# Performance work log

Measured on AMD Instinct MI355X. Metric: run time of the kernel, lower is better.

The kernel has to match this reference:

```python
import jax, jax.numpy as jnp
import numpy as np

B, S, D, H = 8, 4096, 1024, 16
HD = D // H          # 64 head dim
NR = HD // 2         # 32 rotations
BASE = 10000.0


def setup_inputs() -> dict:
    key = jax.random.key(0)
    k0, k1, k2 = jax.random.split(key, 3)
    x = jax.random.normal(k0, (B, S, D), jnp.float32)
    thetas = jax.random.normal(k1, (NR,), jnp.float32) * 0.1
    r_pairs = jax.random.uniform(k2, (NR, 2), jnp.float32) * HD  # float indices in [0, HD)
    theta_scale = jnp.ones((1,), jnp.float32)
    n_rots_scale = jnp.ones((1,), jnp.float32)
    r_matrix = jnp.eye(HD, dtype=jnp.float32)
    inv_freq = 1.0 / (BASE ** (jnp.arange(0, HD, 2, dtype=jnp.float32) / HD))  # [HD/2]
    return {"x": x, "thetas": thetas, "r_pairs": r_pairs,
            "theta_scale": theta_scale, "n_rots_scale": n_rots_scale,
            "r_matrix": r_matrix, "inv_freq": inv_freq}


def reference(x, thetas, r_pairs, theta_scale, n_rots_scale, r_matrix, inv_freq):
    b, s, d = x.shape
    hd = r_matrix.shape[0]
    h = d // hd
    xf = x.reshape(-1, hd)  # [B*S*H, hd]

    # adjusted_n_rots = round(n_rots_scale * n_rots); n_rots_scale == 1 -> all rotations
    # (the int() in torch is non-differentiable/static anyway)
    idx = r_pairs.astype(jnp.int32)          # floor of non-negative floats, like .long()
    th = thetas * theta_scale[0]             # [NR]

    def step(xc, inp):
        i, j, t = inp
        c, sn = jnp.cos(t), jnp.sin(t)
        xi = xc[:, i]
        xj = xc[:, j]
        same = i == j
        # x @ G: col i -> xi*c + xj*s, col j -> -xi*s + xj*c; if i==j torch's
        # overwrite order leaves G[i,i] = cos -> col i = xi*c
        ni = jnp.where(same, xi * c, xi * c + xj * sn)
        nj = jnp.where(same, xi * c, -xi * sn + xj * c)
        xc = xc.at[:, i].set(ni)
        xc = xc.at[:, j].set(nj)
        return xc, None

    xf, _ = jax.lax.scan(step, xf, (idx[:, 0], idx[:, 1], th))
    xf = xf @ r_matrix                       # [B*S*H, hd]
    x4 = xf.reshape(b, s, h, hd)

    pos = jnp.arange(s, dtype=jnp.float32)
    sinusoid = pos[:, None] * inv_freq[None, :]        # [S, hd/2]
    sin = jnp.sin(sinusoid)[None, :, None, :]
    cos = jnp.cos(sinusoid)[None, :, None, :]
    x1 = x4[..., ::2]
    x2 = x4[..., 1::2]
    out = jnp.concatenate([x1 * cos - x2 * sin, x1 * sin + x2 * cos], axis=-1)
    return out.reshape(b, s, d)
```

## Files before the change

### kernel.cpp

```cpp
#include <hip/hip_runtime.h>

#define BB 8
#define SS 4096
#define DD 1024
#define HH 16
#define HD 64
#define NR 32
#define NROWS (BB * SS * HH)
#define NGRP (NROWS / 16)
#define GPW 4
#define GPB (4 * GPW)
#define NBLK (NGRP / GPB)

typedef __attribute__((ext_vector_type(8))) short bf16x8;
typedef __attribute__((ext_vector_type(4))) float f32x4;

__global__ __launch_bounds__(256) void build_pack_kernel(
    const float* __restrict__ thetas,
    const float* __restrict__ r_pairs,
    const float* __restrict__ theta_scale,
    const float* __restrict__ r_matrix,
    unsigned short* __restrict__ Apack)
{
    __shared__ float W[64 * 68];
    __shared__ int   ii[NR], jj[NR];
    __shared__ float cc[NR], ssn[NR];

    const int t = threadIdx.x;

#pragma unroll
    for (int it = 0; it < 16; ++it) {
        int idx = t + 256 * it;
        W[(idx >> 6) * 68 + (idx & 63)] = r_matrix[idx];
    }
    if (t < NR) {
        ii[t] = (int)r_pairs[2 * t];
        jj[t] = (int)r_pairs[2 * t + 1];
        float th = thetas[t] * theta_scale[0];
        cc[t]  = cosf(th);
        ssn[t] = sinf(th);
    }
    __syncthreads();

    if (t < 64) {
        for (int k = NR - 1; k >= 0; --k) {
            int i = ii[k], j = jj[k];
            float c = cc[k], s = ssn[k];
            float xi = W[i * 68 + t];
            float xj = W[j * 68 + t];
            if (i == j) {
                W[i * 68 + t] = c * xi;
            } else {
                W[i * 68 + t] = c * xi - s * xj;
                W[j * 68 + t] = s * xi + c * xj;
            }
        }
    }
    __syncthreads();

#pragma unroll
    for (int it = 0; it < 16; ++it) {
        int flat = t + 256 * it;
        int j    = flat & 7;
        int lane = (flat >> 3) & 63;
        int ks   = (flat >> 9) & 1;
        int tt   = flat >> 10;
        int i    = tt * 16 + (lane & 15);
        int k    = ks * 32 + ((lane >> 4) << 3) + j;
        float v  = W[k * 68 + i];
        unsigned u  = __float_as_uint(v);
        unsigned uh = u & 0xFFFF0000u;
        float fl    = v - __uint_as_float(uh);
        Apack[flat]        = (unsigned short)(uh >> 16);
        Apack[4096 + flat] = (unsigned short)(__float_as_uint(fl) >> 16);
    }
}

__device__ __forceinline__ void split8(const float4 a, const float4 b,
                                       bf16x8& hi, bf16x8& lo)
{
    const float f[8] = {a.x, a.y, a.z, a.w, b.x, b.y, b.z, b.w};
#pragma unroll
    for (int j = 0; j < 8; ++j) {
        unsigned u  = __float_as_uint(f[j]);
        unsigned uh = u & 0xFFFF0000u;
        hi[j] = (short)(uh >> 16);
        float fl = f[j] - __uint_as_float(uh);
        lo[j] = (short)(__float_as_uint(fl) >> 16);
    }
}

__global__ __launch_bounds__(256, 3) void rope_mfma_kernel(
    const float* __restrict__ x,
    const unsigned short* __restrict__ Apack,
    const float* __restrict__ inv_freq,
    float* __restrict__ out)
{
    const int lane = threadIdx.x & 63;
    const int wv   = threadIdx.x >> 6;
    const int q    = lane >> 4;
    const int rr   = lane & 15;

    bf16x8 Ah[4][2], Al[4][2];
    {
        const bf16x8* Ap = (const bf16x8*)Apack;
#pragma unroll
        for (int tt = 0; tt < 4; ++tt)
#pragma unroll
            for (int ks = 0; ks < 2; ++ks) {
                Ah[tt][ks] = Ap[(tt * 2 + ks) * 64 + lane];
                Al[tt][ks] = Ap[512 + (tt * 2 + ks) * 64 + lane];
            }
    }
    float2 invf[4];
#pragma unroll
    for (int tt = 0; tt < 4; ++tt)
        invf[tt] = *(const float2*)&inv_freq[tt * 8 + q * 2];

    int g = blockIdx.x * GPB + wv * GPW;

    const float* xr = x + ((size_t)g * 16 + rr) * 64 + q * 8;
    float4 fa0 = *(const float4*)(xr);
    float4 fa1 = *(const float4*)(xr + 4);
    float4 fa2 = *(const float4*)(xr + 32);
    float4 fa3 = *(const float4*)(xr + 36);

#pragma unroll 1
    for (int gi = 0; gi < GPW; ++gi, ++g) {
        float4 fb0 = fa0, fb1 = fa1, fb2 = fa2, fb3 = fa3;
        if (gi + 1 < GPW) {
            const float* xn = x + ((size_t)(g + 1) * 16 + rr) * 64 + q * 8;
            fb0 = *(const float4*)(xn);
            fb1 = *(const float4*)(xn + 4);
            fb2 = *(const float4*)(xn + 32);
            fb3 = *(const float4*)(xn + 36);
        }

        bf16x8 Bh0, Bl0, Bh1, Bl1;
        split8(fa0, fa1, Bh0, Bl0);
        split8(fa2, fa3, Bh1, Bl1);

        f32x4 acc[4];
#pragma unroll
        for (int tt = 0; tt < 4; ++tt) {
            f32x4 a = {0.f, 0.f, 0.f, 0.f};
            a = __builtin_amdgcn_mfma_f32_16x16x32_bf16(Ah[tt][0], Bh0, a, 0, 0, 0);
            a = __builtin_amdgcn_mfma_f32_16x16x32_bf16(Ah[tt][1], Bh1, a, 0, 0, 0);
            a = __builtin_amdgcn_mfma_f32_16x16x32_bf16(Al[tt][0], Bh0, a, 0, 0, 0);
            a = __builtin_amdgcn_mfma_f32_16x16x32_bf16(Al[tt][1], Bh1, a, 0, 0, 0);
            a = __builtin_amdgcn_mfma_f32_16x16x32_bf16(Ah[tt][0], Bl0, a, 0, 0, 0);
            a = __builtin_amdgcn_mfma_f32_16x16x32_bf16(Ah[tt][1], Bl1, a, 0, 0, 0);
            acc[tt] = a;
        }

        const float pos = (float)(g & (SS - 1));
        float* orow = out + ((size_t)g * 16 + rr) * 64;
#pragma unroll
        for (int tt = 0; tt < 4; ++tt) {
            float sn0, cs0, sn1, cs1;
            __sincosf(pos * invf[tt].x, &sn0, &cs0);
            __sincosf(pos * invf[tt].y, &sn1, &cs1);
            const float y0 = acc[tt][0], y1 = acc[tt][1];
            const float y2 = acc[tt][2], y3 = acc[tt][3];
            const int m0 = tt * 8 + q * 2;
            float2 o1 = { y0 * cs0 - y1 * sn0, y2 * cs1 - y3 * sn1 };
            float2 o2 = { y0 * sn0 + y1 * cs0, y2 * sn1 + y3 * cs1 };
            *(float2*)&orow[m0]      = o1;
            *(float2*)&orow[32 + m0] = o2;
        }

        fa0 = fb0; fa1 = fb1; fa2 = fb2; fa3 = fb3;
    }
}

extern "C" void kernel_launch(void* const* d_in, const int* in_sizes, int n_in,
                              void* d_out, int out_size, void* d_ws, size_t ws_size,
                              hipStream_t stream)
{
    const float* x           = (const float*)d_in[0];
    const float* thetas      = (const float*)d_in[1];
    const float* r_pairs     = (const float*)d_in[2];
    const float* theta_scale = (const float*)d_in[3];
    const float* r_matrix    = (const float*)d_in[5];
    const float* inv_freq    = (const float*)d_in[6];
    float* out = (float*)d_out;
    unsigned short* Apack = (unsigned short*)d_ws;

    build_pack_kernel<<<1, 256, 0, stream>>>(thetas, r_pairs, theta_scale,
                                             r_matrix, Apack);
    rope_mfma_kernel<<<NBLK, 256, 0, stream>>>(x, Apack, inv_freq, out);
}
```

Before: 259.4 us.

## Exchange MFMA outputs across lanes to emit 16-byte nontemporal stores

Lanes in adjacent quads swap accumulator values with a cross-lane shuffle, so each lane holds four consecutive output pairs and writes float4 stores instead of float2 stores. The stores are marked nontemporal to avoid cache pollution on this streaming output, and the occupancy hint rises from 3 to 4 blocks per CU. This halves the number of store instructions and widens each one, at the cost of shuffles and possible register pressure under the tighter launch bound.

Measured after the change: 264.3 us. Within noise of the previous version (+1.9%).

```diff
diff --git a/kernel.cpp b/kernel.cpp
--- a/kernel.cpp
+++ b/kernel.cpp
@@ -90,7 +90,7 @@
     }
 }
 
-__global__ __launch_bounds__(256, 3) void rope_mfma_kernel(
+__global__ __launch_bounds__(256, 4) void rope_mfma_kernel(
     const float* __restrict__ x,
     const unsigned short* __restrict__ Apack,
     const float* __restrict__ inv_freq,
@@ -100,6 +100,9 @@
     const int wv   = threadIdx.x >> 6;
     const int q    = lane >> 4;
     const int rr   = lane & 15;
+    const int qlo  = q & 1;
+    const int qhi  = q >> 1;
+    const bool odd = qlo != 0;
 
     bf16x8 Ah[4][2], Al[4][2];
     {
@@ -112,10 +115,10 @@
                 Al[tt][ks] = Ap[512 + (tt * 2 + ks) * 64 + lane];
             }
     }
-    float2 invf[4];
-#pragma unroll
-    for (int tt = 0; tt < 4; ++tt)
-        invf[tt] = *(const float2*)&inv_freq[tt * 8 + q * 2];
+    float4 invf4[2];
+#pragma unroll
+    for (int pr = 0; pr < 2; ++pr)
+        invf4[pr] = *(const float4*)&inv_freq[8 * qlo + 4 * qhi + 16 * pr];
 
     int g = blockIdx.x * GPB + wv * GPW;
 
@@ -155,18 +158,37 @@
 
         const float pos = (float)(g & (SS - 1));
         float* orow = out + ((size_t)g * 16 + rr) * 64;
-#pragma unroll
-        for (int tt = 0; tt < 4; ++tt) {
-            float sn0, cs0, sn1, cs1;
-            __sincosf(pos * invf[tt].x, &sn0, &cs0);
-            __sincosf(pos * invf[tt].y, &sn1, &cs1);
-            const float y0 = acc[tt][0], y1 = acc[tt][1];
-            const float y2 = acc[tt][2], y3 = acc[tt][3];
-            const int m0 = tt * 8 + q * 2;
-            float2 o1 = { y0 * cs0 - y1 * sn0, y2 * cs1 - y3 * sn1 };
-            float2 o2 = { y0 * sn0 + y1 * cs0, y2 * sn1 + y3 * cs1 };
-            *(float2*)&orow[m0]      = o1;
-            *(float2*)&orow[32 + m0] = o2;
+
+#pragma unroll
+        for (int pr = 0; pr < 2; ++pr) {
+            const f32x4 aE = acc[2 * pr];
+            const f32x4 aO = acc[2 * pr + 1];
+            float y8[8];
+#pragma unroll
+            for (int r = 0; r < 4; ++r) {
+                float send = odd ? aE[r] : aO[r];
+                float recv = __shfl_xor(send, 16, 64);
+                y8[r]     = odd ? recv  : aE[r];
+                y8[4 + r] = odd ? aO[r] : recv;
+            }
+            const float4 fr = invf4[pr];
+            float sn[4], cs[4];
+            __sincosf(pos * fr.x, &sn[0], &cs[0]);
+            __sincosf(pos * fr.y, &sn[1], &cs[1]);
+            __sincosf(pos * fr.z, &sn[2], &cs[2]);
+            __sincosf(pos * fr.w, &sn[3], &cs[3]);
+            f32x4 o1, o2;
+            o1[0] = y8[0] * cs[0] - y8[1] * sn[0];
+            o1[1] = y8[2] * cs[1] - y8[3] * sn[1];
+            o1[2] = y8[4] * cs[2] - y8[5] * sn[2];
+            o1[3] = y8[6] * cs[3] - y8[7] * sn[3];
+            o2[0] = y8[0] * sn[0] + y8[1] * cs[0];
+            o2[1] = y8[2] * sn[1] + y8[3] * cs[1];
+            o2[2] = y8[4] * sn[2] + y8[5] * cs[2];
+            o2[3] = y8[6] * sn[3] + y8[7] * cs[3];
+            const int cb4 = 8 * qlo + 4 * qhi + 16 * pr;
+            __builtin_nontemporal_store(o1, (f32x4*)(orow + cb4));
+            __builtin_nontemporal_store(o2, (f32x4*)(orow + 32 + cb4));
         }
 
         fa0 = fb0; fa1 = fb1; fa2 = fb2; fa3 = fb3;
```
